# Optimization experiments

Hardware: AMD Instinct MI355X
Metric: run time of the kernel (lower is better)

## Reference

```python
import jax, jax.numpy as jnp
import numpy as np

B, C, H, W = 1, 8192, 32, 32
C8 = C // 8  # 1024 == H*W; required by the (b,hw,hw)/(b,c8) broadcast in the original code


def setup_inputs() -> dict:
    key = jax.random.key(0)
    ks = jax.random.split(key, 11)
    rn = lambda i, shape, s=1.0: jax.random.normal(ks[i], shape, dtype=jnp.float32) * s
    return {
        "x": rn(0, (B, C, H, W)),
        "Wq": rn(1, (C8, C), 0.02),
        "Wk": rn(2, (C8, C), 0.02),
        "Wv": rn(3, (C, C), 0.02),
        "q_scale": jax.random.uniform(ks[4], (C8,), minval=0.5, maxval=1.5),
        "q_shift": rn(5, (C8,), 0.1),
        "k_scale": jax.random.uniform(ks[6], (C8,), minval=0.5, maxval=1.5),
        "k_shift": rn(7, (C8,), 0.1),
        "v_scale": jax.random.uniform(ks[8], (C,), minval=0.5, maxval=1.5),
        "v_shift": rn(9, (C,), 0.1),
        "gamma": rn(10, (), 0.5),
    }


def reference(x, Wq, Wk, Wv, q_scale, q_shift, k_scale, k_shift, v_scale, v_shift, gamma):
    b, c, h, w = x.shape
    n = h * w
    xf = x.reshape(b, c, n)  # (b, c, n)
    # BasicConv2d = 1x1 conv (no bias) + BatchNorm2d; BN folded to per-channel scale/shift
    q = jnp.einsum('oc,bcn->bon', Wq, xf) * q_scale[:, None] + q_shift[:, None]  # (b, c8, n)
    k = jnp.einsum('oc,bcn->bon', Wk, xf) * k_scale[:, None] + k_shift[:, None]  # (b, c8, n)
    v = jnp.einsum('oc,bcn->bon', Wv, xf) * v_scale[:, None] + v_shift[:, None]  # (b, c,  n)
    q = q.transpose(0, 2, 1)  # (b, n, c8)
    # PPMCC score: per-channel centering, covariance across channels
    q_c = q - q.mean(axis=1, keepdims=True)
    k_c = k - k.mean(axis=2, keepdims=True)
    cov = jnp.einsum('bnc,bcm->bnm', q_c, k_c) / (n - 1)  # (b, n, n)
    q_std = q.std(axis=1)  # (b, c8), ddof=0 (matches torch unbiased=False)
    k_std = k.std(axis=2)  # (b, c8)
    ppmcc = cov / (q_std * k_std)  # broadcasts over last axis since c8 == n
    att = jax.nn.softmax(ppmcc, axis=-1).transpose(0, 2, 1)  # (b, n, n)
    out = jnp.einsum('bcn,bnm->bcm', v, att).reshape(b, c, h, w)
    return gamma * out + x
```

## Files before the change

kernel.cpp:

```cpp
#include <hip/hip_runtime.h>
#include <cstdint>
#include <cstddef>

#define CDIM 8192
#define NDIM 1024
#define C8D  1024
#define MSTACK 10240
#define NT8 128

typedef __bf16 bf16_t;
typedef __bf16 bf16x8 __attribute__((ext_vector_type(8)));
typedef __bf16 bf16x4 __attribute__((ext_vector_type(4)));
typedef float  f32x4  __attribute__((ext_vector_type(4)));

__device__ __forceinline__ void gload_lds16(const void* g, void* l) {
    __builtin_amdgcn_global_load_lds((const __attribute__((address_space(1))) void*)g,
                                     (__attribute__((address_space(3))) void*)l, 16, 0, 0);
}

__global__ __launch_bounds__(256) void cvt_bf16_k(const float* __restrict__ in,
                                                  bf16_t* __restrict__ out, int n8) {
    int idx = blockIdx.x * 256 + threadIdx.x;
    int stride = gridDim.x * 256;
    for (int i = idx; i < n8; i += stride) {
        size_t off = (size_t)i * 8;
        float4 a = *(const float4*)(in + off);
        float4 b = *(const float4*)(in + off + 4);
        bf16x8 o = { (__bf16)a.x, (__bf16)a.y, (__bf16)a.z, (__bf16)a.w,
                     (__bf16)b.x, (__bf16)b.y, (__bf16)b.z, (__bf16)b.w };
        *(bf16x8*)(out + off) = o;
    }
}

__global__ __launch_bounds__(256) void transpose_cvt_x(const float* __restrict__ x,
                                                       bf16_t* __restrict__ xT) {
    __shared__ float t[32][33];
    const int n0 = blockIdx.x * 32, c0 = blockIdx.y * 32;
    const int tx = threadIdx.x, ty = threadIdx.y;
    #pragma unroll
    for (int i = 0; i < 4; ++i)
        t[ty + i * 8][tx] = x[(size_t)(c0 + ty + i * 8) * NDIM + n0 + tx];
    __syncthreads();
    #pragma unroll
    for (int i = 0; i < 4; ++i)
        xT[(size_t)(n0 + ty + i * 8) * CDIM + c0 + tx] = (__bf16)t[tx][ty + i * 8];
}

__global__ __launch_bounds__(512, 2) void mega_gemm8(
    const bf16_t* __restrict__ Wv, const bf16_t* __restrict__ Wq,
    const bf16_t* __restrict__ Wk, const bf16_t* __restrict__ Bx,
    bf16_t* __restrict__ v_out, float* __restrict__ q_out, float* __restrict__ k_out,
    const float* __restrict__ v_scale, const float* __restrict__ v_shift,
    const float* __restrict__ q_scale, const float* __restrict__ q_shift,
    const float* __restrict__ k_scale, const float* __restrict__ k_shift)
{
    __shared__ __align__(16) bf16_t Ld[65536];

    const int tid  = threadIdx.x;
    const int lane = tid & 63;
    const int wid  = tid >> 6;
    const int wr   = wid >> 2;
    const int wc   = wid & 3;

    const int lin  = blockIdx.y * 4 + blockIdx.x;
    const int tile = (lin & 7) * 20 + (lin >> 3);
    const int trow = tile >> 2;
    const int col0 = (tile & 3) * 256;

    const bf16_t* Ag; const float* s0; const float* s1; int arow, path;
    if (trow < 32)      { Ag = Wv; arow = trow * 256;        s0 = v_scale; s1 = v_shift; path = 0; }
    else if (trow < 36) { Ag = Wq; arow = trow * 256 - 8192; s0 = q_scale; s1 = q_shift; path = 1; }
    else                { Ag = Wk; arow = trow * 256 - 9216; s0 = k_scale; s1 = k_shift; path = 2; }

    const int ar0 = tid >> 3;
    const int o0  = tid * 8;
    const int csw = (((tid & 7) ^ ((tid >> 3) & 7)) << 3);

    const int lr   = lane & 15;
    const int hi8  = (lane >> 4) * 8;
    const int rsw  = (lane & 7) << 3;
    const int ck0  = hi8 ^ rsw;
    const int ck1  = (32 + hi8) ^ rsw;
    const int aRow = wr * 64 + lr;
    const int bRow = wc * 32 + lr;

    bf16x8 av[4][2];
    bf16x8 bv[2][2][2];
    f32x4  acc[2][2][4][2];
    #pragma unroll
    for (int mh = 0; mh < 2; ++mh)
        #pragma unroll
        for (int nh = 0; nh < 2; ++nh)
            #pragma unroll
            for (int fi = 0; fi < 4; ++fi)
                #pragma unroll
                for (int fj = 0; fj < 2; ++fj)
                    acc[mh][nh][fi][fj] = (f32x4){0.f, 0.f, 0.f, 0.f};

#define STAGE_AH(BUF, H, KB) do {                                                             \
    gload_lds16(Ag + (size_t)(arow + (H)*128 + ar0     ) * CDIM + (KB) + csw,                 \
                Ld + (BUF)*16384 + (H)*8192 + o0);                                            \
    gload_lds16(Ag + (size_t)(arow + (H)*128 + ar0 + 64) * CDIM + (KB) + csw,                 \
                Ld + (BUF)*16384 + (H)*8192 + o0 + 4096);                                     \
} while (0)

#define STAGE_BH(BUF, H, KB) do {                                                             \
    gload_lds16(Bx + (size_t)(col0 + (H)*128 + ar0     ) * CDIM + (KB) + csw,                 \
                Ld + 32768 + (BUF)*16384 + (H)*8192 + o0);                                    \
    gload_lds16(Bx + (size_t)(col0 + (H)*128 + ar0 + 64) * CDIM + (KB) + csw,                 \
                Ld + 32768 + (BUF)*16384 + (H)*8192 + o0 + 4096);                             \
} while (0)

#define RD_A(BUF, MH) do {                                                                    \
    _Pragma("unroll") for (int fi = 0; fi < 4; ++fi) {                                        \
        av[fi][0] = *(const bf16x8*)(Ld + (BUF)*16384 + ((MH)*128 + aRow + fi*16)*64 + ck0);  \
        av[fi][1] = *(const bf16x8*)(Ld + (BUF)*16384 + ((MH)*128 + aRow + fi*16)*64 + ck1);  \
    }                                                                                         \
} while (0)

#define RD_B(BUF, NH) do {                                                                    \
    _Pragma("unroll") for (int fj = 0; fj < 2; ++fj) {                                        \
        bv[NH][fj][0] = *(const bf16x8*)(Ld + 32768 + (BUF)*16384 +                           \
                                         ((NH)*128 + bRow + fj*16)*64 + ck0);                 \
        bv[NH][fj][1] = *(const bf16x8*)(Ld + 32768 + (BUF)*16384 +                           \
                                         ((NH)*128 + bRow + fj*16)*64 + ck1);                 \
    }                                                                                         \
} while (0)

#define MMA(MH, NH) do {                                                                      \
    __builtin_amdgcn_s_setprio(1);                                                            \
    _Pragma("unroll") for (int kk = 0; kk < 2; ++kk)                                          \
        _Pragma("unroll") for (int fi = 0; fi < 4; ++fi)                                      \
            _Pragma("unroll") for (int fj = 0; fj < 2; ++fj)                                  \
                acc[MH][NH][fi][fj] = __builtin_amdgcn_mfma_f32_16x16x32_bf16(                \
                    av[fi][kk], bv[NH][fj][kk], acc[MH][NH][fi][fj], 0, 0, 0);                \
    __builtin_amdgcn_s_setprio(0);                                                            \
} while (0)

#define SYNC_TOP do {                                                                         \
    __builtin_amdgcn_s_barrier();                                                             \
    asm volatile("s_waitcnt lgkmcnt(0)" ::: "memory");                                        \
    __builtin_amdgcn_sched_barrier(0);                                                        \
} while (0)

#define SYNC_END do {                                                                         \
    __builtin_amdgcn_s_barrier();                                                             \
} while (0)

#define KTILE(BUF, T, DO_S2, VM) do {                                                         \
                                                                          \
    RD_A(BUF, 0); RD_B(BUF, 0);                                                               \
    if ((T) + 1 < NT8) STAGE_BH((BUF)^1, 1, ((T)+1)*64);                                      \
    SYNC_TOP; MMA(0, 0); SYNC_END;                                                            \
                                                                          \
    RD_B(BUF, 1);                                                                             \
    if (DO_S2) STAGE_AH(BUF, 0, ((T)+2)*64);                                                  \
    SYNC_TOP; MMA(0, 1); SYNC_END;                                                            \
                                                                          \
    RD_A(BUF, 1);                                                                             \
    if (DO_S2) STAGE_BH(BUF, 0, ((T)+2)*64);                                                  \
    SYNC_TOP; MMA(1, 1); SYNC_END;                                                            \
                                                         \
    if (DO_S2) STAGE_AH(BUF, 1, ((T)+2)*64);                                                  \
    SYNC_TOP; MMA(1, 0);                                                                      \
    if ((VM) == 6)      { asm volatile("s_waitcnt vmcnt(6)" ::: "memory");                    \
                          __builtin_amdgcn_sched_barrier(0); }                                \
    else if ((VM) == 0) { asm volatile("s_waitcnt vmcnt(0)" ::: "memory");                    \
                          __builtin_amdgcn_sched_barrier(0); }                                \
    SYNC_END;                                                                                 \
} while (0)

    STAGE_AH(0, 0, 0); STAGE_BH(0, 0, 0); STAGE_AH(0, 1, 0); STAGE_BH(0, 1, 0);
    STAGE_AH(1, 0, 64); STAGE_BH(1, 0, 64); STAGE_AH(1, 1, 64);
    asm volatile("s_waitcnt vmcnt(6)" ::: "memory");
    __builtin_amdgcn_sched_barrier(0);
    __builtin_amdgcn_s_barrier();

    for (int t = 0; t < NT8 - 2; t += 2) {
        KTILE(0, t,     1, 6);
        KTILE(1, t + 1, 1, 6);
    }
    KTILE(0, NT8 - 2, 0, 0);
    KTILE(1, NT8 - 1, 0, -1);

#undef KTILE
#undef SYNC_END
#undef SYNC_TOP
#undef MMA
#undef RD_B
#undef RD_A
#undef STAGE_BH
#undef STAGE_AH

    const int cq = (lane >> 4) * 4;
    #pragma unroll
    for (int mh = 0; mh < 2; ++mh) {
        #pragma unroll
        for (int nh = 0; nh < 2; ++nh) {
            #pragma unroll
            for (int fi = 0; fi < 4; ++fi) {
                #pragma unroll
                for (int fj = 0; fj < 2; ++fj) {
                    const int j = col0 + nh * 128 + wc * 32 + fj * 16 + lr;
                    #pragma unroll
                    for (int r = 0; r < 4; ++r) {
                        const int il = arow + mh * 128 + wr * 64 + fi * 16 + cq + r;
                        float vv = acc[mh][nh][fi][fj][r] * s0[il] + s1[il];
                        if (path == 0)      v_out[(size_t)il * NDIM + j] = (__bf16)vv;
                        else if (path == 1) q_out[(size_t)il * NDIM + j] = vv;
                        else                k_out[(size_t)il * NDIM + j] = vv;
                    }
                }
            }
        }
    }
}

template <int EPI, typename OutT>
__global__ __launch_bounds__(256) void gemm_bt(
    const bf16_t* __restrict__ A, const bf16_t* __restrict__ B,
    OutT* __restrict__ C, int M, int N, int K,
    const float* __restrict__ e0, const float* __restrict__ e1,
    const float* __restrict__ gs)
{
    const int gx = gridDim.x;
    const int nwg = gx * gridDim.y;
    const int lin = blockIdx.y * gx + blockIdx.x;
    int tile = lin;
    if ((nwg & 7) == 0) tile = (lin & 7) * (nwg >> 3) + (lin >> 3);
    const int row0 = (tile / gx) * 128;
    const int col0 = (tile % gx) * 128;

    const int Ks  = K / gridDim.z;
    const int kb0 = blockIdx.z * Ks;
    const int kb1 = kb0 + Ks;
    OutT* Cz = C + (size_t)blockIdx.z * M * N;

    const int tid = threadIdx.x;
    __shared__ __align__(16) bf16_t As[2 * 4096];
    __shared__ __align__(16) bf16_t Bs[2 * 4096];

    const int lane = tid & 63;
    const int w    = tid >> 6;
    const int wm   = (w >> 1) * 64;
    const int wn   = (w & 1) * 64;
    const int lr   = lane & 15;
    const int kg   = (lane >> 4) * 8;

    f32x4 acc[4][4];
    #pragma unroll
    for (int a_ = 0; a_ < 4; ++a_)
        #pragma unroll
        for (int b_ = 0; b_ < 4; ++b_)
            acc[a_][b_] = (f32x4){0.f, 0.f, 0.f, 0.f};

    const int eA = tid * 8;
    const int eB = (256 + tid) * 8;
    const int rA = eA >> 5, cA = eA & 31;
    const int rB = eB >> 5, cB = eB & 31;

#define BT_STAGE(buf, kb)                                                       \
    do {                                                                        \
        gload_lds16(A + (size_t)(row0 + rA) * K + (kb) + cA, As + (buf)*4096 + eA); \
        gload_lds16(A + (size_t)(row0 + rB) * K + (kb) + cB, As + (buf)*4096 + eB); \
        gload_lds16(B + (size_t)(col0 + rA) * K + (kb) + cA, Bs + (buf)*4096 + eA); \
        gload_lds16(B + (size_t)(col0 + rB) * K + (kb) + cB, Bs + (buf)*4096 + eB); \
    } while (0)

    BT_STAGE(0, kb0);
    __syncthreads();
    int cur = 0;
    for (int kb = kb0; kb < kb1; kb += 32) {
        if (kb + 32 < kb1) BT_STAGE(cur ^ 1, kb + 32);
        const bf16_t* Ac = As + cur * 4096;
        const bf16_t* Bc = Bs + cur * 4096;

        bf16x8 av[4], bv[4];
        #pragma unroll
        for (int mi = 0; mi < 4; ++mi)
            av[mi] = *(const bf16x8*)(Ac + (wm + mi * 16 + lr) * 32 + kg);
        #pragma unroll
        for (int ni = 0; ni < 4; ++ni)
            bv[ni] = *(const bf16x8*)(Bc + (wn + ni * 16 + lr) * 32 + kg);

        #pragma unroll
        for (int mi = 0; mi < 4; ++mi)
            #pragma unroll
            for (int ni = 0; ni < 4; ++ni)
                acc[mi][ni] = __builtin_amdgcn_mfma_f32_16x16x32_bf16(
                    av[mi], bv[ni], acc[mi][ni], 0, 0, 0);
        __syncthreads();
        cur ^= 1;
    }
#undef BT_STAGE

    float g = 0.f;
    if (EPI == 3) g = gs[0];
    const int cr = (lane >> 4) * 4;
    #pragma unroll
    for (int mi = 0; mi < 4; ++mi) {
        #pragma unroll
        for (int ni = 0; ni < 4; ++ni) {
            const int j = col0 + wn + ni * 16 + lr;
            float s0 = 0.f, s1 = 0.f;
            if (EPI == 2) { s0 = e0[j]; s1 = e1[j]; }
            #pragma unroll
            for (int r = 0; r < 4; ++r) {
                const int i = row0 + wm + mi * 16 + cr + r;
                float v = acc[mi][ni][r];
                if (EPI == 2)      v = v * (1.0f / 1023.0f) / (s0 * s1);
                else if (EPI == 3) v = g * v + e0[(size_t)i * N + j];
                Cz[(size_t)i * N + j] = (OutT)v;
            }
        }
    }
}

__global__ __launch_bounds__(256) void rowstats(
    const float* __restrict__ Q, const float* __restrict__ Km,
    float* __restrict__ qmean, float* __restrict__ qstd,
    float* __restrict__ kmean, float* __restrict__ kstd)
{
    const int wid  = blockIdx.x * 4 + (threadIdx.x >> 6);
    const int lane = threadIdx.x & 63;
    const float* src = (wid < 1024) ? (Q + (size_t)wid * NDIM)
                                    : (Km + (size_t)(wid - 1024) * NDIM);
    float s = 0.f, s2 = 0.f;
    #pragma unroll
    for (int p = 0; p < 4; ++p) {
        float4 v = *(const float4*)(src + p * 256 + lane * 4);
        s  += v.x + v.y + v.z + v.w;
        s2 += v.x * v.x + v.y * v.y + v.z * v.z + v.w * v.w;
    }
    #pragma unroll
    for (int o = 32; o; o >>= 1) { s += __shfl_xor(s, o); s2 += __shfl_xor(s2, o); }
    if (lane == 0) {
        float m   = s / 1024.f;
        float var = fmaxf(s2 / 1024.f - m * m, 0.f);
        if (wid < 1024) { qmean[wid] = m; qstd[wid] = sqrtf(var); }
        else            { kmean[wid - 1024] = m; kstd[wid - 1024] = sqrtf(var); }
    }
}

__global__ __launch_bounds__(256) void center_tr(
    const float* __restrict__ Q, const float* __restrict__ qmu, bf16_t* __restrict__ qc,
    const float* __restrict__ Km, const float* __restrict__ kmu, bf16_t* __restrict__ kc)
{
    __shared__ float t[32][33];
    const float* M  = blockIdx.z ? Km  : Q;
    const float* mu = blockIdx.z ? kmu : qmu;
    bf16_t* O       = blockIdx.z ? kc  : qc;
    const int o0 = blockIdx.y * 32, n0 = blockIdx.x * 32;
    const int tx = threadIdx.x, ty = threadIdx.y;
    #pragma unroll
    for (int i = 0; i < 4; ++i) {
        const int o = o0 + ty + i * 8;
        t[ty + i * 8][tx] = M[(size_t)o * NDIM + n0 + tx] - mu[o];
    }
    __syncthreads();
    #pragma unroll
    for (int i = 0; i < 4; ++i)
        O[(size_t)(n0 + ty + i * 8) * C8D + o0 + tx] = (__bf16)t[tx][ty + i * 8];
}

__global__ __launch_bounds__(256) void softmax_rows(const float* __restrict__ P,
                                                    bf16_t* __restrict__ O) {
    const int row = blockIdx.x;
    const int tid = threadIdx.x;
    const size_t PL = (size_t)NDIM * NDIM / 4;
    const size_t u  = (size_t)row * (NDIM / 4) + tid;
    const float4* B = (const float4*)P;
    float4 p0 = B[u], p1 = B[u + PL], p2 = B[u + 2 * PL], p3 = B[u + 3 * PL];
    float4 v = { p0.x + p1.x + p2.x + p3.x, p0.y + p1.y + p2.y + p3.y,
                 p0.z + p1.z + p2.z + p3.z, p0.w + p1.w + p2.w + p3.w };
    float mx = fmaxf(fmaxf(v.x, v.y), fmaxf(v.z, v.w));
    #pragma unroll
    for (int o = 32; o; o >>= 1) mx = fmaxf(mx, __shfl_xor(mx, o));
    __shared__ float red[8];
    const int w = tid >> 6, lane = tid & 63;
    if (lane == 0) red[w] = mx;
    __syncthreads();
    mx = fmaxf(fmaxf(red[0], red[1]), fmaxf(red[2], red[3]));
    float e0 = __expf(v.x - mx), e1 = __expf(v.y - mx);
    float e2 = __expf(v.z - mx), e3 = __expf(v.w - mx);
    float s = e0 + e1 + e2 + e3;
    #pragma unroll
    for (int o = 32; o; o >>= 1) s += __shfl_xor(s, o);
    if (lane == 0) red[4 + w] = s;
    __syncthreads();
    s = red[4] + red[5] + red[6] + red[7];
    const float inv = 1.0f / s;
    bf16x4 o4 = { (__bf16)(e0 * inv), (__bf16)(e1 * inv),
                  (__bf16)(e2 * inv), (__bf16)(e3 * inv) };
    ((bf16x4*)(O + (size_t)row * NDIM))[tid] = o4;
}

extern "C" void kernel_launch(void* const* d_in, const int* in_sizes, int n_in,
                              void* d_out, int out_size, void* d_ws, size_t ws_size,
                              hipStream_t stream)
{
    const float* x       = (const float*)d_in[0];
    const float* Wq      = (const float*)d_in[1];
    const float* Wk      = (const float*)d_in[2];
    const float* Wv      = (const float*)d_in[3];
    const float* q_scale = (const float*)d_in[4];
    const float* q_shift = (const float*)d_in[5];
    const float* k_scale = (const float*)d_in[6];
    const float* k_shift = (const float*)d_in[7];
    const float* v_scale = (const float*)d_in[8];
    const float* v_shift = (const float*)d_in[9];
    const float* gamma   = (const float*)d_in[10];
    float* out = (float*)d_out;

    char* w = (char*)d_ws;
    bf16_t* Wv_b = (bf16_t*)w; w += (size_t)CDIM * CDIM * 2;
    bf16_t* Wq_b = (bf16_t*)w; w += (size_t)C8D  * CDIM * 2;
    bf16_t* Wk_b = (bf16_t*)w; w += (size_t)C8D  * CDIM * 2;
    bf16_t* xT   = (bf16_t*)w; w += (size_t)NDIM * CDIM * 2;
    bf16_t* v_b  = (bf16_t*)w; w += (size_t)CDIM * NDIM * 2;
    float*  q_on = (float*) w; w += (size_t)C8D * NDIM * 4;
    float*  k_on = (float*) w; w += (size_t)C8D * NDIM * 4;
    float*  P    = (float*) w; w += (size_t)4 * NDIM * NDIM * 4;
    bf16_t* qc   = (bf16_t*)w; w += (size_t)NDIM * C8D * 2;
    bf16_t* kc   = (bf16_t*)w; w += (size_t)NDIM * C8D * 2;
    bf16_t* A0   = (bf16_t*)w; w += (size_t)NDIM * NDIM * 2;
    float*  qmean = (float*)w; w += C8D * 4;
    float*  qstd  = (float*)w; w += C8D * 4;
    float*  kmean = (float*)w; w += C8D * 4;
    float*  kstd  = (float*)w; w += C8D * 4;

    cvt_bf16_k<<<2048, 256, 0, stream>>>(Wv, Wv_b, (int)((size_t)CDIM * CDIM / 8));
    cvt_bf16_k<<<2048, 256, 0, stream>>>(Wq, Wq_b, C8D * CDIM / 8);
    cvt_bf16_k<<<2048, 256, 0, stream>>>(Wk, Wk_b, C8D * CDIM / 8);
    transpose_cvt_x<<<dim3(NDIM / 32, CDIM / 32), dim3(32, 8), 0, stream>>>(x, xT);

    mega_gemm8<<<dim3(4, MSTACK / 256), 512, 0, stream>>>(
        Wv_b, Wq_b, Wk_b, xT, v_b, q_on, k_on,
        v_scale, v_shift, q_scale, q_shift, k_scale, k_shift);

    rowstats<<<512, 256, 0, stream>>>(q_on, k_on, qmean, qstd, kmean, kstd);

    center_tr<<<dim3(32, 32, 2), dim3(32, 8), 0, stream>>>(
        q_on, qmean, qc, k_on, kmean, kc);

    gemm_bt<2, float><<<dim3(NDIM / 128, NDIM / 128, 4), 256, 0, stream>>>(
        qc, kc, P, NDIM, NDIM, C8D, qstd, kstd, nullptr);

    softmax_rows<<<NDIM, 256, 0, stream>>>(P, A0);

    gemm_bt<3, float><<<dim3(NDIM / 128, CDIM / 128, 1), 256, 0, stream>>>(
        v_b, A0, out, CDIM, NDIM, NDIM, x, x, gamma);
}
```

Baseline: 355.3 us.

## Fuse fp32-to-bf16 weight conversion into the projection GEMM's A-tile loads

```diff
diff --git a/kernel.cpp b/kernel.cpp
--- a/kernel.cpp
+++ b/kernel.cpp
@@ -18,20 +18,6 @@
                                      (__attribute__((address_space(3))) void*)l, 16, 0, 0);
 }
 
-__global__ __launch_bounds__(256) void cvt_bf16_k(const float* __restrict__ in,
-                                                  bf16_t* __restrict__ out, int n8) {
-    int idx = blockIdx.x * 256 + threadIdx.x;
-    int stride = gridDim.x * 256;
-    for (int i = idx; i < n8; i += stride) {
-        size_t off = (size_t)i * 8;
-        float4 a = *(const float4*)(in + off);
-        float4 b = *(const float4*)(in + off + 4);
-        bf16x8 o = { (__bf16)a.x, (__bf16)a.y, (__bf16)a.z, (__bf16)a.w,
-                     (__bf16)b.x, (__bf16)b.y, (__bf16)b.z, (__bf16)b.w };
-        *(bf16x8*)(out + off) = o;
-    }
-}
-
 __global__ __launch_bounds__(256) void transpose_cvt_x(const float* __restrict__ x,
                                                        bf16_t* __restrict__ xT) {
     __shared__ float t[32][33];
@@ -47,8 +33,8 @@
 }
 
 __global__ __launch_bounds__(512, 2) void mega_gemm8(
-    const bf16_t* __restrict__ Wv, const bf16_t* __restrict__ Wq,
-    const bf16_t* __restrict__ Wk, const bf16_t* __restrict__ Bx,
+    const float* __restrict__ Wv, const float* __restrict__ Wq,
+    const float* __restrict__ Wk, const bf16_t* __restrict__ Bx,
     bf16_t* __restrict__ v_out, float* __restrict__ q_out, float* __restrict__ k_out,
     const float* __restrict__ v_scale, const float* __restrict__ v_shift,
     const float* __restrict__ q_scale, const float* __restrict__ q_shift,
@@ -67,7 +53,7 @@
     const int trow = tile >> 2;
     const int col0 = (tile & 3) * 256;
 
-    const bf16_t* Ag; const float* s0; const float* s1; int arow, path;
+    const float* Ag; const float* s0; const float* s1; int arow, path;
     if (trow < 32)      { Ag = Wv; arow = trow * 256;        s0 = v_scale; s1 = v_shift; path = 0; }
     else if (trow < 36) { Ag = Wq; arow = trow * 256 - 8192; s0 = q_scale; s1 = q_shift; path = 1; }
     else                { Ag = Wk; arow = trow * 256 - 9216; s0 = k_scale; s1 = k_shift; path = 2; }
@@ -75,6 +61,11 @@
     const int ar0 = tid >> 3;
     const int o0  = tid * 8;
     const int csw = (((tid & 7) ^ ((tid >> 3) & 7)) << 3);
+
+    const int aqr = tid >> 2;
+    const int aqc = (tid & 3) * 16;
+    const int ag1 = ((tid & 3) * 2)     ^ (aqr & 7);
+    const int ag2 = ((tid & 3) * 2 + 1) ^ (aqr & 7);
 
     const int lr   = lane & 15;
     const int hi8  = (lane >> 4) * 8;
@@ -87,6 +78,7 @@
     bf16x8 av[4][2];
     bf16x8 bv[2][2][2];
     f32x4  acc[2][2][4][2];
+    float4 regsA0[4], regsA1[4];
     #pragma unroll
     for (int mh = 0; mh < 2; ++mh)
         #pragma unroll
@@ -97,18 +89,29 @@
                 for (int fj = 0; fj < 2; ++fj)
                     acc[mh][nh][fi][fj] = (f32x4){0.f, 0.f, 0.f, 0.f};
 
-#define STAGE_AH(BUF, H, KB) do {                                                             \
-    gload_lds16(Ag + (size_t)(arow + (H)*128 + ar0     ) * CDIM + (KB) + csw,                 \
-                Ld + (BUF)*16384 + (H)*8192 + o0);                                            \
-    gload_lds16(Ag + (size_t)(arow + (H)*128 + ar0 + 64) * CDIM + (KB) + csw,                 \
-                Ld + (BUF)*16384 + (H)*8192 + o0 + 4096);                                     \
-} while (0)
-
 #define STAGE_BH(BUF, H, KB) do {                                                             \
     gload_lds16(Bx + (size_t)(col0 + (H)*128 + ar0     ) * CDIM + (KB) + csw,                 \
                 Ld + 32768 + (BUF)*16384 + (H)*8192 + o0);                                    \
     gload_lds16(Bx + (size_t)(col0 + (H)*128 + ar0 + 64) * CDIM + (KB) + csw,                 \
                 Ld + 32768 + (BUF)*16384 + (H)*8192 + o0 + 4096);                             \
+} while (0)
+
+#define A_ISSUE(REGS, H, KB) do {                                                             \
+    const float* ap_ = Ag + (size_t)(arow + (H)*128 + aqr) * CDIM + (KB) + aqc;               \
+    REGS[0] = *(const float4*)(ap_);                                                          \
+    REGS[1] = *(const float4*)(ap_ + 4);                                                      \
+    REGS[2] = *(const float4*)(ap_ + 8);                                                      \
+    REGS[3] = *(const float4*)(ap_ + 12);                                                     \
+} while (0)
+
+#define A_WRITE(REGS, BUF, H) do {                                                            \
+    bf16_t* wb_ = Ld + (BUF)*16384 + (H)*8192 + aqr*64;                                       \
+    bf16x8 w0_ = { (__bf16)REGS[0].x, (__bf16)REGS[0].y, (__bf16)REGS[0].z, (__bf16)REGS[0].w,\
+                   (__bf16)REGS[1].x, (__bf16)REGS[1].y, (__bf16)REGS[1].z, (__bf16)REGS[1].w };\
+    bf16x8 w1_ = { (__bf16)REGS[2].x, (__bf16)REGS[2].y, (__bf16)REGS[2].z, (__bf16)REGS[2].w,\
+                   (__bf16)REGS[3].x, (__bf16)REGS[3].y, (__bf16)REGS[3].z, (__bf16)REGS[3].w };\
+    *(bf16x8*)(wb_ + ag1 * 8) = w0_;                                                          \
+    *(bf16x8*)(wb_ + ag2 * 8) = w1_;                                                          \
 } while (0)
 
 #define RD_A(BUF, MH) do {                                                                    \
@@ -137,60 +140,89 @@
     __builtin_amdgcn_s_setprio(0);                                                            \
 } while (0)
 
-#define SYNC_TOP do {                                                                         \
-    __builtin_amdgcn_s_barrier();                                                             \
-    asm volatile("s_waitcnt lgkmcnt(0)" ::: "memory");                                        \
-    __builtin_amdgcn_sched_barrier(0);                                                        \
-} while (0)
-
-#define SYNC_END do {                                                                         \
-    __builtin_amdgcn_s_barrier();                                                             \
-} while (0)
-
-#define KTILE(BUF, T, DO_S2, VM) do {                                                         \
-                                                                          \
-    RD_A(BUF, 0); RD_B(BUF, 0);                                                               \
-    if ((T) + 1 < NT8) STAGE_BH((BUF)^1, 1, ((T)+1)*64);                                      \
-    SYNC_TOP; MMA(0, 0); SYNC_END;                                                            \
-                                                                          \
-    RD_B(BUF, 1);                                                                             \
-    if (DO_S2) STAGE_AH(BUF, 0, ((T)+2)*64);                                                  \
-    SYNC_TOP; MMA(0, 1); SYNC_END;                                                            \
-                                                                          \
-    RD_A(BUF, 1);                                                                             \
-    if (DO_S2) STAGE_BH(BUF, 0, ((T)+2)*64);                                                  \
-    SYNC_TOP; MMA(1, 1); SYNC_END;                                                            \
-                                                         \
-    if (DO_S2) STAGE_AH(BUF, 1, ((T)+2)*64);                                                  \
-    SYNC_TOP; MMA(1, 0);                                                                      \
-    if ((VM) == 6)      { asm volatile("s_waitcnt vmcnt(6)" ::: "memory");                    \
-                          __builtin_amdgcn_sched_barrier(0); }                                \
-    else if ((VM) == 0) { asm volatile("s_waitcnt vmcnt(0)" ::: "memory");                    \
-                          __builtin_amdgcn_sched_barrier(0); }                                \
-    SYNC_END;                                                                                 \
-} while (0)
-
-    STAGE_AH(0, 0, 0); STAGE_BH(0, 0, 0); STAGE_AH(0, 1, 0); STAGE_BH(0, 1, 0);
-    STAGE_AH(1, 0, 64); STAGE_BH(1, 0, 64); STAGE_AH(1, 1, 64);
+#define LGKM0 do { asm volatile("s_waitcnt lgkmcnt(0)" ::: "memory");                         \
+                   __builtin_amdgcn_sched_barrier(0); } while (0)
+#define BAR   __builtin_amdgcn_s_barrier()
+
+    A_ISSUE(regsA0, 0, 0);
+    A_ISSUE(regsA1, 1, 0);
+    STAGE_BH(0, 0, 0);
+    STAGE_BH(0, 1, 0);
+    asm volatile("s_waitcnt vmcnt(4)" ::: "memory");
+    __builtin_amdgcn_sched_barrier(0);
+    A_WRITE(regsA0, 0, 0);
+    A_WRITE(regsA1, 0, 1);
+    A_ISSUE(regsA0, 0, 64);
+    STAGE_BH(1, 0, 64);
+    A_ISSUE(regsA1, 1, 64);
     asm volatile("s_waitcnt vmcnt(6)" ::: "memory");
     __builtin_amdgcn_sched_barrier(0);
-    __builtin_amdgcn_s_barrier();
+    A_WRITE(regsA0, 1, 0);
+    LGKM0;
+    BAR;
+
+#define KTILE_F(BUF, T) do {                                                                  \
+                                                                                      \
+    RD_A(BUF, 0); RD_B(BUF, 0);                                                               \
+    STAGE_BH((BUF)^1, 1, ((T)+1)*64);                                                         \
+    BAR; LGKM0; MMA(0, 0); BAR;                                                               \
+                                                                                      \
+    RD_B(BUF, 1);                                                                             \
+    A_ISSUE(regsA0, 0, ((T)+2)*64);                                                           \
+    asm volatile("s_waitcnt vmcnt(6)" ::: "memory");                                          \
+    __builtin_amdgcn_sched_barrier(0);                                                        \
+    A_WRITE(regsA1, (BUF)^1, 1);                                                              \
+    LGKM0; BAR; MMA(0, 1); BAR;                                                               \
+                                                                                      \
+    RD_A(BUF, 1);                                                                             \
+    STAGE_BH(BUF, 0, ((T)+2)*64);                                                             \
+    BAR; LGKM0; MMA(1, 1); BAR;                                                               \
+                                                                                      \
+    A_ISSUE(regsA1, 1, ((T)+2)*64);                                                           \
+    asm volatile("s_waitcnt vmcnt(6)" ::: "memory");                                          \
+    __builtin_amdgcn_sched_barrier(0);                                                        \
+    A_WRITE(regsA0, BUF, 0);                                                                  \
+    LGKM0; BAR; MMA(1, 0); BAR;                                                               \
+} while (0)
 
     for (int t = 0; t < NT8 - 2; t += 2) {
-        KTILE(0, t,     1, 6);
-        KTILE(1, t + 1, 1, 6);
-    }
-    KTILE(0, NT8 - 2, 0, 0);
-    KTILE(1, NT8 - 1, 0, -1);
-
-#undef KTILE
-#undef SYNC_END
-#undef SYNC_TOP
+        KTILE_F(0, t);
+        KTILE_F(1, t + 1);
+    }
+    {
+        RD_A(0, 0); RD_B(0, 0);
+        STAGE_BH(1, 1, (NT8 - 1) * 64);
+        BAR; LGKM0; MMA(0, 0); BAR;
+        RD_B(0, 1);
+        asm volatile("s_waitcnt vmcnt(2)" ::: "memory");
+        __builtin_amdgcn_sched_barrier(0);
+        A_WRITE(regsA1, 1, 1);
+        LGKM0; BAR; MMA(0, 1); BAR;
+        RD_A(0, 1);
+        BAR; LGKM0; MMA(1, 1); BAR;
+        asm volatile("s_waitcnt vmcnt(0)" ::: "memory");
+        __builtin_amdgcn_sched_barrier(0);
+        BAR; LGKM0; MMA(1, 0); BAR;
+    }
+    {
+        RD_A(1, 0); RD_B(1, 0);
+        BAR; LGKM0; MMA(0, 0); BAR;
+        RD_B(1, 1);
+        BAR; LGKM0; MMA(0, 1); BAR;
+        RD_A(1, 1);
+        BAR; LGKM0; MMA(1, 1); BAR;
+        LGKM0; MMA(1, 0);
+    }
+
+#undef KTILE_F
+#undef BAR
+#undef LGKM0
 #undef MMA
 #undef RD_B
 #undef RD_A
+#undef A_WRITE
+#undef A_ISSUE
 #undef STAGE_BH
-#undef STAGE_AH
 
     const int cq = (lane >> 4) * 4;
     #pragma unroll
@@ -413,9 +445,6 @@
     float* out = (float*)d_out;
 
     char* w = (char*)d_ws;
-    bf16_t* Wv_b = (bf16_t*)w; w += (size_t)CDIM * CDIM * 2;
-    bf16_t* Wq_b = (bf16_t*)w; w += (size_t)C8D  * CDIM * 2;
-    bf16_t* Wk_b = (bf16_t*)w; w += (size_t)C8D  * CDIM * 2;
     bf16_t* xT   = (bf16_t*)w; w += (size_t)NDIM * CDIM * 2;
     bf16_t* v_b  = (bf16_t*)w; w += (size_t)CDIM * NDIM * 2;
     float*  q_on = (float*) w; w += (size_t)C8D * NDIM * 4;
@@ -429,13 +458,10 @@
     float*  kmean = (float*)w; w += C8D * 4;
     float*  kstd  = (float*)w; w += C8D * 4;
 
-    cvt_bf16_k<<<2048, 256, 0, stream>>>(Wv, Wv_b, (int)((size_t)CDIM * CDIM / 8));
-    cvt_bf16_k<<<2048, 256, 0, stream>>>(Wq, Wq_b, C8D * CDIM / 8);
-    cvt_bf16_k<<<2048, 256, 0, stream>>>(Wk, Wk_b, C8D * CDIM / 8);
     transpose_cvt_x<<<dim3(NDIM / 32, CDIM / 32), dim3(32, 8), 0, stream>>>(x, xT);
 
     mega_gemm8<<<dim3(4, MSTACK / 256), 512, 0, stream>>>(
-        Wv_b, Wq_b, Wk_b, xT, v_b, q_on, k_on,
+        Wv, Wq, Wk, xT, v_b, q_on, k_on,
         v_scale, v_shift, q_scale, q_shift, k_scale, k_shift);
 
     rowstats<<<512, 256, 0, stream>>>(q_on, k_on, qmean, qstd, kmean, kstd);
```

Result: slower. 518.1 us (+45.8%).
